# Kernel optimization log

Measured on AMD Instinct MI355X. Metric: run time of the kernel, lower is better.

Reference implementation:

```python
import jax, jax.numpy as jnp
import numpy as np

KERNEL = 3
PAD = (KERNEL - 1) // 2  # non-causal symmetric padding


def setup_inputs() -> dict:
    key = jax.random.key(0)
    k1, k2, k3 = jax.random.split(key, 3)
    B, Cin, Cout, S = 16, 64, 64, 1024
    return {
        "input": jax.random.normal(k1, (B, Cin, S), dtype=jnp.float32),
        "weight": jax.random.normal(k2, (Cout, Cin, S, KERNEL), dtype=jnp.float32),
        "bias": jax.random.normal(k3, (Cout, S), dtype=jnp.float32),
    }


def reference(input, weight, bias):
    # input: (B, Cin, S); weight: (Cout, Cin, S, K); bias: (Cout, S)
    S = input.shape[-1]
    padded = jnp.pad(input, ((0, 0), (0, 0), (PAD, PAD)))
    # unfolded windows: (B, Cin, S, K) -- small, avoids the (B,Cout,Cin,S,K) blowup
    unfolded = jnp.stack([padded[:, :, k:k + S] for k in range(KERNEL)], axis=-1)
    # position-specific (non-weight-shared) conv: contract Cin and K per position s
    out = jnp.einsum("bcsk,ocsk->bos", unfolded, weight)
    return out + bias[None, :, :]
```

## Files before the change

### kernel.cpp

```cpp
#include <hip/hip_runtime.h>

namespace {
constexpr int CIN = 64, COUT = 64, SS = 1024, KK = 3;
constexpr int STL = 4;
constexpr int POS = STL + 2;
constexpr int NCG = 8, CPG = 8;
}

__global__ __launch_bounds__(512)
void locon1d(const float* __restrict__ in, const float* __restrict__ wt,
             const float* __restrict__ bias, float* __restrict__ out) {
  __shared__ float smem[8192];

  const int tid = threadIdx.x;
  const int sl  = tid & 3;
  const int og  = (tid >> 2) & 15;
  const int cg  = tid >> 6;
  const int bid = blockIdx.x;
  const int st  = ((bid & 7) << 5) + (bid >> 3);
  const int s0  = st * STL;
  const int s   = s0 + sl;
  const int o0  = og * 4;
  const int cb  = cg * CPG;

  #pragma unroll
  for (int i = 0; i < 3; ++i) {
    const int t  = tid + i * 512;
    const int c  = t / 24;
    const int r  = t - c * 24;
    const int bq = r / 6;
    const int p  = r - bq * 6;
    const int sg = s0 - 1 + p;
    const bool v = (unsigned)sg < (unsigned)SS;
    const float* ip = in + ((size_t)(4 * bq) * CIN + c) * SS + sg;
    float4 x4;
    x4.x = v ? ip[0] : 0.f;
    x4.y = v ? ip[(size_t)1 * CIN * SS] : 0.f;
    x4.z = v ? ip[(size_t)2 * CIN * SS] : 0.f;
    x4.w = v ? ip[(size_t)3 * CIN * SS] : 0.f;
    *reinterpret_cast<float4*>(&smem[(c * POS + p) * 16 + 4 * bq]) = x4;
  }
  __syncthreads();

  const float* wbase = wt + ((size_t)o0 * CIN + cb) * (SS * KK) + (size_t)s * KK;

  float acc[4][16];
  #pragma unroll
  for (int oo = 0; oo < 4; ++oo)
    #pragma unroll
    for (int b = 0; b < 16; ++b) acc[oo][b] = 0.f;

  float wA[4][3], wB[4][3], wC[4][3];

  #define WLD(DST, C_) do {                                                    \
    _Pragma("unroll")                                                          \
    for (int oo = 0; oo < 4; ++oo)                                             \
      _Pragma("unroll")                                                        \
      for (int k = 0; k < KK; ++k)                                             \
        DST[oo][k] = wbase[(size_t)oo * (CIN * SS * KK) +                      \
                           (size_t)(C_) * (SS * KK) + k];                      \
  } while (0)

  #define CMP(W, C_) do {                                                      \
    _Pragma("unroll")                                                          \
    for (int k = 0; k < KK; ++k) {                                             \
      const float* base_ = &smem[((cb + (C_)) * POS + sl + k) * 16];           \
      _Pragma("unroll")                                                        \
      for (int g = 0; g < 4; ++g) {                                            \
        const float4 x4 = *reinterpret_cast<const float4*>(base_ + 4 * g);     \
        _Pragma("unroll")                                                      \
        for (int oo = 0; oo < 4; ++oo) {                                       \
          const float wv = W[oo][k];                                           \
          acc[oo][4 * g + 0] += wv * x4.x;                                     \
          acc[oo][4 * g + 1] += wv * x4.y;                                     \
          acc[oo][4 * g + 2] += wv * x4.z;                                     \
          acc[oo][4 * g + 3] += wv * x4.w;                                     \
        }                                                                      \
      }                                                                        \
    }                                                                          \
  } while (0)

  WLD(wA, 0); WLD(wB, 1); WLD(wC, 2);
  CMP(wA, 0); WLD(wA, 3);
  CMP(wB, 1); WLD(wB, 4);
  CMP(wC, 2); WLD(wC, 5);
  CMP(wA, 3); WLD(wA, 6);
  CMP(wB, 4); WLD(wB, 7);
  CMP(wC, 5);
  CMP(wA, 6);
  CMP(wB, 7);

  #undef WLD
  #undef CMP

  #pragma unroll
  for (int oo = 0; oo < 4; ++oo) {
    __syncthreads();
    #pragma unroll
    for (int b = 0; b < 16; ++b)
      smem[cg * 1024 + (b * 16 + og) * 4 + sl] = acc[oo][b];
    __syncthreads();
    #pragma unroll
    for (int i = 0; i < 2; ++i) {
      const int item = tid + i * 512;
      float sum = 0.f;
      #pragma unroll
      for (int g = 0; g < NCG; ++g) sum += smem[g * 1024 + item];
      const int b   = item >> 6;
      const int rem = item & 63;
      const int o   = (rem >> 2) * 4 + oo;
      const int s2  = s0 + (rem & 3);
      out[((size_t)b * COUT + o) * SS + s2] = sum + bias[o * SS + s2];
    }
  }
}

extern "C" void kernel_launch(void* const* d_in, const int* in_sizes, int n_in,
                              void* d_out, int out_size, void* d_ws, size_t ws_size,
                              hipStream_t stream) {
  const float* in = (const float*)d_in[0];
  const float* wt = (const float*)d_in[1];
  const float* bs = (const float*)d_in[2];
  float* out = (float*)d_out;
  hipLaunchKernelGGL(locon1d, dim3(256), dim3(512), 0, stream, in, wt, bs, out);
}
```

Measured before the change: 99.61 us.

## Split batch across blocks, deepen per-thread channel chain, single-pass swizzled reduction

The grid doubles to 512 blocks of 256 threads. Each block now handles 8 of the 16 batches, and each thread covers 16 input channels instead of 8, so there are 4 channel groups instead of 8. The first weight loads are issued before the input staging and its barrier, to hide load latency. The cross-group reduction now runs as one pass through a swizzled shared-memory layout instead of four synchronized rounds, which cuts barriers and bank conflicts. In exchange, every weight element is fetched by two blocks, one per batch half, which relies on cache hits to avoid doubling DRAM weight traffic.

```diff
diff --git a/kernel.cpp b/kernel.cpp
--- a/kernel.cpp
+++ b/kernel.cpp
@@ -4,10 +4,11 @@
 constexpr int CIN = 64, COUT = 64, SS = 1024, KK = 3;
 constexpr int STL = 4;
 constexpr int POS = STL + 2;
-constexpr int NCG = 8, CPG = 8;
+constexpr int NCG = 4, CPG = 16;
+constexpr int BB  = 8;
 }
 
-__global__ __launch_bounds__(512)
+__global__ __launch_bounds__(256)
 void locon1d(const float* __restrict__ in, const float* __restrict__ wt,
              const float* __restrict__ bias, float* __restrict__ out) {
   __shared__ float smem[8192];
@@ -17,38 +18,16 @@
   const int og  = (tid >> 2) & 15;
   const int cg  = tid >> 6;
   const int bid = blockIdx.x;
-  const int st  = ((bid & 7) << 5) + (bid >> 3);
+  const int p   = bid & 255;
+  const int h   = bid >> 8;
+  const int st  = ((p & 7) << 5) + (p >> 3);
   const int s0  = st * STL;
   const int s   = s0 + sl;
   const int o0  = og * 4;
   const int cb  = cg * CPG;
-
-  #pragma unroll
-  for (int i = 0; i < 3; ++i) {
-    const int t  = tid + i * 512;
-    const int c  = t / 24;
-    const int r  = t - c * 24;
-    const int bq = r / 6;
-    const int p  = r - bq * 6;
-    const int sg = s0 - 1 + p;
-    const bool v = (unsigned)sg < (unsigned)SS;
-    const float* ip = in + ((size_t)(4 * bq) * CIN + c) * SS + sg;
-    float4 x4;
-    x4.x = v ? ip[0] : 0.f;
-    x4.y = v ? ip[(size_t)1 * CIN * SS] : 0.f;
-    x4.z = v ? ip[(size_t)2 * CIN * SS] : 0.f;
-    x4.w = v ? ip[(size_t)3 * CIN * SS] : 0.f;
-    *reinterpret_cast<float4*>(&smem[(c * POS + p) * 16 + 4 * bq]) = x4;
-  }
-  __syncthreads();
+  const int b0  = h * BB;
 
   const float* wbase = wt + ((size_t)o0 * CIN + cb) * (SS * KK) + (size_t)s * KK;
-
-  float acc[4][16];
-  #pragma unroll
-  for (int oo = 0; oo < 4; ++oo)
-    #pragma unroll
-    for (int b = 0; b < 16; ++b) acc[oo][b] = 0.f;
 
   float wA[4][3], wB[4][3], wC[4][3];
 
@@ -61,12 +40,39 @@
                            (size_t)(C_) * (SS * KK) + k];                      \
   } while (0)
 
+  WLD(wA, 0); WLD(wB, 1); WLD(wC, 2);
+
+  #pragma unroll
+  for (int i = 0; i < 3; ++i) {
+    const int t  = tid + i * 256;
+    const int c  = t / 12;
+    const int r  = t - c * 12;
+    const int bq = r / 6;
+    const int pp = r - bq * 6;
+    const int sg = s0 - 1 + pp;
+    const bool v = (unsigned)sg < (unsigned)SS;
+    const float* ip = in + ((size_t)(b0 + 4 * bq) * CIN + c) * SS + sg;
+    float4 x4;
+    x4.x = v ? ip[0] : 0.f;
+    x4.y = v ? ip[(size_t)1 * CIN * SS] : 0.f;
+    x4.z = v ? ip[(size_t)2 * CIN * SS] : 0.f;
+    x4.w = v ? ip[(size_t)3 * CIN * SS] : 0.f;
+    *reinterpret_cast<float4*>(&smem[(c * POS + pp) * 8 + 4 * bq]) = x4;
+  }
+  __syncthreads();
+
+  float acc[4][BB];
+  #pragma unroll
+  for (int oo = 0; oo < 4; ++oo)
+    #pragma unroll
+    for (int b = 0; b < BB; ++b) acc[oo][b] = 0.f;
+
   #define CMP(W, C_) do {                                                      \
     _Pragma("unroll")                                                          \
     for (int k = 0; k < KK; ++k) {                                             \
-      const float* base_ = &smem[((cb + (C_)) * POS + sl + k) * 16];           \
+      const float* base_ = &smem[((cb + (C_)) * POS + sl + k) * 8];            \
       _Pragma("unroll")                                                        \
-      for (int g = 0; g < 4; ++g) {                                            \
+      for (int g = 0; g < 2; ++g) {                                            \
         const float4 x4 = *reinterpret_cast<const float4*>(base_ + 4 * g);     \
         _Pragma("unroll")                                                      \
         for (int oo = 0; oo < 4; ++oo) {                                       \
@@ -80,38 +86,47 @@
     }                                                                          \
   } while (0)
 
-  WLD(wA, 0); WLD(wB, 1); WLD(wC, 2);
-  CMP(wA, 0); WLD(wA, 3);
-  CMP(wB, 1); WLD(wB, 4);
-  CMP(wC, 2); WLD(wC, 5);
-  CMP(wA, 3); WLD(wA, 6);
-  CMP(wB, 4); WLD(wB, 7);
-  CMP(wC, 5);
-  CMP(wA, 6);
-  CMP(wB, 7);
+  CMP(wA,  0); WLD(wA,  3);
+  CMP(wB,  1); WLD(wB,  4);
+  CMP(wC,  2); WLD(wC,  5);
+  CMP(wA,  3); WLD(wA,  6);
+  CMP(wB,  4); WLD(wB,  7);
+  CMP(wC,  5); WLD(wC,  8);
+  CMP(wA,  6); WLD(wA,  9);
+  CMP(wB,  7); WLD(wB, 10);
+  CMP(wC,  8); WLD(wC, 11);
+  CMP(wA,  9); WLD(wA, 12);
+  CMP(wB, 10); WLD(wB, 13);
+  CMP(wC, 11); WLD(wC, 14);
+  CMP(wA, 12); WLD(wA, 15);
+  CMP(wB, 13);
+  CMP(wC, 14);
+  CMP(wA, 15);
 
   #undef WLD
   #undef CMP
 
+  __syncthreads();
   #pragma unroll
-  for (int oo = 0; oo < 4; ++oo) {
-    __syncthreads();
+  for (int oo = 0; oo < 4; ++oo)
     #pragma unroll
-    for (int b = 0; b < 16; ++b)
-      smem[cg * 1024 + (b * 16 + og) * 4 + sl] = acc[oo][b];
-    __syncthreads();
+    for (int bb = 0; bb < BB; ++bb) {
+      const int e = bb * 256 + (og * 4 + oo) * 4 + sl;
+      smem[cg * 2048 + (e ^ (((e >> 5) & 7) << 2))] = acc[oo][bb];
+    }
+  __syncthreads();
+  #pragma unroll
+  for (int i = 0; i < 8; ++i) {
+    const int item = tid + i * 256;
+    const int sw   = item ^ (((item >> 5) & 7) << 2);
+    float sum = 0.f;
     #pragma unroll
-    for (int i = 0; i < 2; ++i) {
-      const int item = tid + i * 512;
-      float sum = 0.f;
-      #pragma unroll
-      for (int g = 0; g < NCG; ++g) sum += smem[g * 1024 + item];
-      const int b   = item >> 6;
-      const int rem = item & 63;
-      const int o   = (rem >> 2) * 4 + oo;
-      const int s2  = s0 + (rem & 3);
-      out[((size_t)b * COUT + o) * SS + s2] = sum + bias[o * SS + s2];
-    }
+    for (int g = 0; g < NCG; ++g) sum += smem[g * 2048 + sw];
+    const int bl  = item >> 8;
+    const int rem = item & 255;
+    const int o   = rem >> 2;
+    const int s2  = s0 + (rem & 3);
+    out[((size_t)(b0 + bl) * COUT + o) * SS + s2] = sum + bias[o * SS + s2];
   }
 }
 
@@ -122,5 +137,5 @@
   const float* wt = (const float*)d_in[1];
   const float* bs = (const float*)d_in[2];
   float* out = (float*)d_out;
-  hipLaunchKernelGGL(locon1d, dim3(256), dim3(512), 0, stream, in, wt, bs, out);
+  hipLaunchKernelGGL(locon1d, dim3(512), dim3(256), 0, stream, in, wt, bs, out);
 }
```

New measurement: 110.0 us. 1.1x slower.

## Stage inputs per wave, hoist weight loads, single-pass swizzled LDS reduction

Applied to the files above, without the earlier changes.

Each wave now stages only the input channels for its own channel group into LDS. This removes the block-wide barrier before compute, and the first weight loads are issued before the input loads. The cross-channel-group reduction changes from four sync-heavy passes into one pass, using a separate, much larger LDS partials region with an XOR swizzle to reduce bank conflicts. Bias is prefetched into registers. The LDS footprint grows to about 155 KB, which limits each CU to one block and relies on in-wave LDS ordering for correctness.

```diff
diff --git a/kernel.cpp b/kernel.cpp
--- a/kernel.cpp
+++ b/kernel.cpp
@@ -5,50 +5,29 @@
 constexpr int STL = 4;
 constexpr int POS = STL + 2;
 constexpr int NCG = 8, CPG = 8;
+constexpr int XS_DW   = CIN * POS * 16;
+constexpr int PART_DW = NCG * 4096;
+constexpr int SMEMDW  = XS_DW + PART_DW;
 }
 
 __global__ __launch_bounds__(512)
 void locon1d(const float* __restrict__ in, const float* __restrict__ wt,
              const float* __restrict__ bias, float* __restrict__ out) {
-  __shared__ float smem[8192];
+  __shared__ float smem[SMEMDW];
 
-  const int tid = threadIdx.x;
-  const int sl  = tid & 3;
-  const int og  = (tid >> 2) & 15;
-  const int cg  = tid >> 6;
-  const int bid = blockIdx.x;
+  const int tid  = threadIdx.x;
+  const int sl   = tid & 3;
+  const int og   = (tid >> 2) & 15;
+  const int cg   = tid >> 6;
+  const int lane = tid & 63;
+  const int bid  = blockIdx.x;
   const int st  = ((bid & 7) << 5) + (bid >> 3);
   const int s0  = st * STL;
   const int s   = s0 + sl;
   const int o0  = og * 4;
   const int cb  = cg * CPG;
 
-  #pragma unroll
-  for (int i = 0; i < 3; ++i) {
-    const int t  = tid + i * 512;
-    const int c  = t / 24;
-    const int r  = t - c * 24;
-    const int bq = r / 6;
-    const int p  = r - bq * 6;
-    const int sg = s0 - 1 + p;
-    const bool v = (unsigned)sg < (unsigned)SS;
-    const float* ip = in + ((size_t)(4 * bq) * CIN + c) * SS + sg;
-    float4 x4;
-    x4.x = v ? ip[0] : 0.f;
-    x4.y = v ? ip[(size_t)1 * CIN * SS] : 0.f;
-    x4.z = v ? ip[(size_t)2 * CIN * SS] : 0.f;
-    x4.w = v ? ip[(size_t)3 * CIN * SS] : 0.f;
-    *reinterpret_cast<float4*>(&smem[(c * POS + p) * 16 + 4 * bq]) = x4;
-  }
-  __syncthreads();
-
   const float* wbase = wt + ((size_t)o0 * CIN + cb) * (SS * KK) + (size_t)s * KK;
-
-  float acc[4][16];
-  #pragma unroll
-  for (int oo = 0; oo < 4; ++oo)
-    #pragma unroll
-    for (int b = 0; b < 16; ++b) acc[oo][b] = 0.f;
 
   float wA[4][3], wB[4][3], wC[4][3];
 
@@ -60,6 +39,33 @@
         DST[oo][k] = wbase[(size_t)oo * (CIN * SS * KK) +                      \
                            (size_t)(C_) * (SS * KK) + k];                      \
   } while (0)
+
+  WLD(wA, 0); WLD(wB, 1); WLD(wC, 2);
+
+  #pragma unroll
+  for (int i = 0; i < 3; ++i) {
+    const int t  = lane + i * 64;
+    const int cl = t / 24;
+    const int r  = t - cl * 24;
+    const int bq = r / 6;
+    const int p  = r - bq * 6;
+    const int c  = cb + cl;
+    const int sg = s0 - 1 + p;
+    const bool v = (unsigned)sg < (unsigned)SS;
+    const float* ip = in + ((size_t)(4 * bq) * CIN + c) * SS + sg;
+    float4 x4;
+    x4.x = v ? ip[0] : 0.f;
+    x4.y = v ? ip[(size_t)1 * CIN * SS] : 0.f;
+    x4.z = v ? ip[(size_t)2 * CIN * SS] : 0.f;
+    x4.w = v ? ip[(size_t)3 * CIN * SS] : 0.f;
+    *reinterpret_cast<float4*>(&smem[(c * POS + p) * 16 + 4 * bq]) = x4;
+  }
+
+  float acc[4][16];
+  #pragma unroll
+  for (int oo = 0; oo < 4; ++oo)
+    #pragma unroll
+    for (int b = 0; b < 16; ++b) acc[oo][b] = 0.f;
 
   #define CMP(W, C_) do {                                                      \
     _Pragma("unroll")                                                          \
@@ -80,7 +86,6 @@
     }                                                                          \
   } while (0)
 
-  WLD(wA, 0); WLD(wB, 1); WLD(wC, 2);
   CMP(wA, 0); WLD(wA, 3);
   CMP(wB, 1); WLD(wB, 4);
   CMP(wC, 2); WLD(wC, 5);
@@ -93,25 +98,34 @@
   #undef WLD
   #undef CMP
 
+  float bz[8];
   #pragma unroll
-  for (int oo = 0; oo < 4; ++oo) {
-    __syncthreads();
+  for (int i = 0; i < 8; ++i) {
+    const int item = tid + i * 512;
+    const int o    = (item >> 2) & 63;
+    const int s2   = s0 + (item & 3);
+    bz[i] = bias[o * SS + s2];
+  }
+
+  #pragma unroll
+  for (int oo = 0; oo < 4; ++oo)
     #pragma unroll
-    for (int b = 0; b < 16; ++b)
-      smem[cg * 1024 + (b * 16 + og) * 4 + sl] = acc[oo][b];
-    __syncthreads();
+    for (int b = 0; b < 16; ++b) {
+      const int A = b * 256 + (og * 4 + oo) * 4 + sl;
+      smem[XS_DW + cg * 4096 + (A ^ (((A >> 5) & 7) << 2))] = acc[oo][b];
+    }
+  __syncthreads();
+  #pragma unroll
+  for (int i = 0; i < 8; ++i) {
+    const int item = tid + i * 512;
+    const int sw   = item ^ (((item >> 5) & 7) << 2);
+    float sum = 0.f;
     #pragma unroll
-    for (int i = 0; i < 2; ++i) {
-      const int item = tid + i * 512;
-      float sum = 0.f;
-      #pragma unroll
-      for (int g = 0; g < NCG; ++g) sum += smem[g * 1024 + item];
-      const int b   = item >> 6;
-      const int rem = item & 63;
-      const int o   = (rem >> 2) * 4 + oo;
-      const int s2  = s0 + (rem & 3);
-      out[((size_t)b * COUT + o) * SS + s2] = sum + bias[o * SS + s2];
-    }
+    for (int g = 0; g < NCG; ++g) sum += smem[XS_DW + g * 4096 + sw];
+    const int b   = item >> 8;
+    const int o   = (item >> 2) & 63;
+    const int s2  = s0 + (item & 3);
+    out[((size_t)b * COUT + o) * SS + s2] = sum + bz[i];
   }
 }
 
```

Measured after the change: 94.17 us. 1.06x faster.
